# Performance work log

Measured on AMD Instinct MI355X. Metric: run time of the kernel, lower is better.

The kernel has to match this reference:

```python
import jax, jax.numpy as jnp
import numpy as np

B, L, P, K, D, H = 8192, 224, 6, 5, 128, 4
S = K * K                 # 25 spatial positions in the patch
CENTER = S // 2           # central target pixel index
SCALE_RANGE = 0.2
BN_EPS = 1e-5


def _uniform(k, shape, fan_in):
    s = 1.0 / np.sqrt(fan_in)
    return jax.random.uniform(k, shape, jnp.float32, -s, s)


def setup_inputs() -> dict:
    key = jax.random.key(0)
    ks = jax.random.split(key, 32)
    inp = {}
    inp["x"] = jax.random.normal(ks[0], (B, L, K, K), jnp.float32)
    # attention projections (stored as (in, out), applied as x @ W + b)
    inp["wk_w"] = _uniform(ks[1], (L, D), L); inp["wk_b"] = _uniform(ks[2], (D,), L)
    inp["wv_w"] = _uniform(ks[3], (L, D), L); inp["wv_b"] = _uniform(ks[4], (D,), L)
    inp["wq_w"] = _uniform(ks[5], (L, D), L); inp["wq_b"] = _uniform(ks[6], (D,), L)
    inp["ng_w"] = _uniform(ks[7], (D, 1), D); inp["ng_b"] = _uniform(ks[8], (1,), D)
    # ffn branch: GLU(128->64) -> BN -> GLU(64->P)
    inp["f1_fw"] = _uniform(ks[9], (D, 64), D);  inp["f1_fb"] = _uniform(ks[10], (64,), D)
    inp["f1_gw"] = _uniform(ks[11], (D, 64), D); inp["f1_gb"] = _uniform(ks[12], (64,), D)
    inp["f_bn_g"] = jnp.ones((64,), jnp.float32); inp["f_bn_b"] = jnp.zeros((64,), jnp.float32)
    inp["f2_fw"] = _uniform(ks[13], (64, P), 64); inp["f2_fb"] = _uniform(ks[14], (P,), 64)
    inp["f2_gw"] = _uniform(ks[15], (64, P), 64); inp["f2_gb"] = _uniform(ks[16], (P,), 64)
    # scalar branch: same shapes
    inp["s1_fw"] = _uniform(ks[17], (D, 64), D);  inp["s1_fb"] = _uniform(ks[18], (64,), D)
    inp["s1_gw"] = _uniform(ks[19], (D, 64), D);  inp["s1_gb"] = _uniform(ks[20], (64,), D)
    inp["s_bn_g"] = jnp.ones((64,), jnp.float32); inp["s_bn_b"] = jnp.zeros((64,), jnp.float32)
    inp["s2_fw"] = _uniform(ks[21], (64, P), 64); inp["s2_fb"] = _uniform(ks[22], (P,), 64)
    inp["s2_gw"] = _uniform(ks[23], (64, P), 64); inp["s2_gb"] = _uniform(ks[24], (P,), 64)
    # endmember spectra (P, L), nonnegative as typical for HSI
    inp["endmember"] = jax.random.uniform(ks[25], (P, L), jnp.float32)
    return inp


def _swish(x):
    return x * jax.nn.sigmoid(x)


def _glu(x, fw, fb, gw, gb):
    return (x @ fw + fb) * jax.nn.sigmoid(x @ gw + gb)


def _bn_train(x, g, b):
    # BatchNorm1d training-mode forward: biased batch stats over batch dim
    m = jnp.mean(x, axis=0)
    v = jnp.var(x, axis=0)
    return (x - m) * jax.lax.rsqrt(v + BN_EPS) * g + b


def _forward(x, wk_w, wk_b, wv_w, wv_b, wq_w, wq_b, ng_w, ng_b,
             f1_fw, f1_fb, f1_gw, f1_gb, f_bn_g, f_bn_b, f2_fw, f2_fb, f2_gw, f2_gb,
             s1_fw, s1_fb, s1_gw, s1_gb, s_bn_g, s_bn_b, s2_fw, s2_fb, s2_gw, s2_gb,
             endmember):
    b = x.shape[0]
    xt = x.reshape(b, L, S).transpose(0, 2, 1)        # (B, S, L)
    keys = xt @ wk_w + wk_b                            # (B, S, D)
    vals = xt @ wv_w + wv_b                            # (B, S, D)
    q = xt[:, CENTER] @ wq_w + wq_b                    # (B, D)
    dk, dv = D // H, D // H
    kh = keys.reshape(b, S, H, dk)
    qh = q.reshape(b, H, dk)
    # note: scaling uses full key_dim (np.sqrt(self.key_dim)), not per-head dim
    scores = jnp.einsum('bhd,bshd->bhs', qh, kh) / np.sqrt(D).astype(np.float32)
    mask = jnp.zeros((S,), jnp.float32).at[CENTER].set(-1e6)
    att = jax.nn.softmax(scores + mask, axis=-1)       # (B, H, S)
    vh = vals.reshape(b, S, H, dv)
    surround = jnp.einsum('bhs,bshd->bhd', att, vh).reshape(b, D)
    central = vals[:, CENTER]                          # (B, D)
    nearby = jax.nn.sigmoid((central - surround) @ ng_w + ng_b)  # (B, 1)
    ss = central + nearby * surround                   # (B, D) spatial-spectral feature

    h = _glu(_swish(ss), f1_fw, f1_fb, f1_gw, f1_gb)
    h = _swish(_bn_train(h, f_bn_g, f_bn_b))
    abd = jax.nn.softmax(_glu(h, f2_fw, f2_fb, f2_gw, f2_gb), axis=1)  # (B, P)

    g = _glu(_swish(ss), s1_fw, s1_fb, s1_gw, s1_gb)
    g = _swish(_bn_train(g, s_bn_g, s_bn_b))
    edm_scale = jnp.tanh(_glu(g, s2_fw, s2_fb, s2_gw, s2_gb))          # (B, P)

    scale = 1.0 + SCALE_RANGE * edm_scale[:, :, None]  # (B, P, 1)
    edm = scale * endmember[None]                      # (B, P, L)
    recon = jnp.einsum('bp,bpl->bl', abd, edm)         # (B, L)
    return recon, abd, edm_scale


def reference(x, wk_w, wk_b, wv_w, wv_b, wq_w, wq_b, ng_w, ng_b,
              f1_fw, f1_fb, f1_gw, f1_gb, f_bn_g, f_bn_b, f2_fw, f2_fb, f2_gw, f2_gb,
              s1_fw, s1_fb, s1_gw, s1_gb, s_bn_g, s_bn_b, s2_fw, s2_fb, s2_gw, s2_gb,
              endmember):
    return _forward(x, wk_w, wk_b, wv_w, wv_b, wq_w, wq_b, ng_w, ng_b,
                    f1_fw, f1_fb, f1_gw, f1_gb, f_bn_g, f_bn_b, f2_fw, f2_fb, f2_gw, f2_gb,
                    s1_fw, s1_fb, s1_gw, s1_gb, s_bn_g, s_bn_b, s2_fw, s2_fb, s2_gw, s2_gb,
                    endmember)
```

## Files before the change

kernel.cpp:

```cpp
#include <hip/hip_runtime.h>
#include <hip/hip_bf16.h>

typedef unsigned short ushort;
typedef unsigned int   uint;
typedef __bf16 bfrag_t __attribute__((ext_vector_type(8)));
typedef float  ffrag_t __attribute__((ext_vector_type(4)));

#define NB   8192
#define LL   224
#define SS   25
#define CTR  12
#define DD   128
#define PP   6
#define HID  64
#define GPB  2
#define NKC  7
#define NMT  4
#define NNT  24
#define VST  132
#define WPK_ELEMS (NKC * NNT * 64 * 8)
#define FC1_ELEMS (4 * 16 * 64 * 8)

__device__ __forceinline__ float f_sigmoid(float x) { return 1.0f / (1.0f + __expf(-x)); }
__device__ __forceinline__ ushort f2bf(float f) {
    __hip_bfloat16 h = __float2bfloat16(f);
    ushort u; __builtin_memcpy(&u, &h, 2); return u;
}
__device__ __forceinline__ float bfu2f(ushort u) {
    uint v = ((uint)u) << 16; float f; __builtin_memcpy(&f, &v, 4); return f;
}

__global__ __launch_bounds__(256) void k0_pack(
    const float* __restrict__ wk_w, const float* __restrict__ wv_w,
    const float* __restrict__ wq_w,
    const float* __restrict__ f1_fw, const float* __restrict__ f1_gw,
    const float* __restrict__ s1_fw, const float* __restrict__ s1_gw,
    ushort* __restrict__ wpack, ushort* __restrict__ fc1pack,
    float* __restrict__ stats)
{
    const int blk = blockIdx.x;
    if (blk == 0) stats[threadIdx.x] = 0.f;
    if (blk < NNT) {
        const int nt  = blk;
        const int mat = nt >> 3;
        const float* w = mat == 0 ? wk_w : (mat == 1 ? wv_w : wq_w);
        const int cb = (nt & 7) * 16;
        for (int e = threadIdx.x; e < NKC * 64 * 8; e += 256) {
            int j    = e & 7;
            int lane = (e >> 3) & 63;
            int kc   = e >> 9;
            int k = kc * 32 + ((lane >> 4) << 3) + j;
            int c = cb + (lane & 15);
            wpack[((kc * NNT + nt) * 64 + lane) * 8 + j] = f2bf(w[k * DD + c]);
        }
    } else {
        const int nt = blk - NNT;
        const int m2 = nt >> 2;
        const float* w = m2 == 0 ? f1_fw : (m2 == 1 ? f1_gw : (m2 == 2 ? s1_fw : s1_gw));
        const int cb = (nt & 3) * 16;
        for (int e = threadIdx.x; e < 4 * 64 * 8; e += 256) {
            int j    = e & 7;
            int lane = (e >> 3) & 63;
            int kc   = e >> 9;
            int k = kc * 32 + ((lane >> 4) << 3) + j;
            int c = cb + (lane & 15);
            fc1pack[((kc * 16 + nt) * 64 + lane) * 8 + j] = f2bf(w[k * HID + c]);
        }
    }
}

__global__ __launch_bounds__(512, 4) void kA_front(
    const float* __restrict__ x,
    const ushort* __restrict__ wpack,
    const float* __restrict__ wk_b, const float* __restrict__ wv_b,
    const float* __restrict__ wq_b,
    const float* __restrict__ ng_w, const float* __restrict__ ng_b,
    ushort* __restrict__ swv_ws)
{
    __shared__ ushort alds[NMT * NKC * 64 * 8];
    __shared__ float  qv[GPB * DD];
    __shared__ float  att[8 * 26];
    __shared__ float  red[4];

    const int t    = threadIdx.x;
    const int b0   = blockIdx.x * GPB;
    const int wave = t >> 6;
    const int lane = t & 63;

    const int cC = wave * 16 + (lane & 15);
    const float biask = wk_b[cC];
    const float biasv = wv_b[cC];
    const float biasq = wq_b[cC];
    const float ngw   = ng_w[t & 127];

    const float4* xb4 = (const float4*)(x + (size_t)b0 * (LL * SS));
    float4 xf[6];
#pragma unroll
    for (int k = 0; k < 6; ++k) {
        int q = t + k * 512;
        if (q < 2800) xf[k] = xb4[q];
    }
#pragma unroll
    for (int k = 0; k < 6; ++k) {
        int q = t + k * 512;
        if (q < 2800) {
            int e0 = q * 4;
            int g  = e0 >= 5600;
            int eb0 = e0 - g * 5600;
#pragma unroll
            for (int c = 0; c < 4; ++c) {
                int eb = eb0 + c;
                int l = eb / 25;
                int s = eb - l * 25;
                int r = g * 32 + s;
                int idx = (((r >> 4) * NKC + (l >> 5)) * 64 +
                           ((r & 15) | (((l >> 3) & 3) << 4))) * 8 + (l & 7);
                float fv = c == 0 ? xf[k].x : c == 1 ? xf[k].y : c == 2 ? xf[k].z : xf[k].w;
                alds[idx] = f2bf(fv);
            }
        }
    }
    __syncthreads();

    ffrag_t acck[NMT], accv[NMT], accq[2];
#pragma unroll
    for (int mt = 0; mt < NMT; ++mt) {
        acck[mt] = ffrag_t{0.f, 0.f, 0.f, 0.f};
        accv[mt] = ffrag_t{0.f, 0.f, 0.f, 0.f};
    }
    accq[0] = ffrag_t{0.f, 0.f, 0.f, 0.f};
    accq[1] = ffrag_t{0.f, 0.f, 0.f, 0.f};

    bfrag_t bk = *(const bfrag_t*)(wpack + ((0 * NNT + wave) * 64 + lane) * 8);
    bfrag_t bv = *(const bfrag_t*)(wpack + ((0 * NNT + wave + 8) * 64 + lane) * 8);
    bfrag_t bq = *(const bfrag_t*)(wpack + ((0 * NNT + wave + 16) * 64 + lane) * 8);
#pragma unroll
    for (int kc = 0; kc < NKC; ++kc) {
        bfrag_t nbk, nbv, nbq;
        if (kc + 1 < NKC) {
            nbk = *(const bfrag_t*)(wpack + (((kc + 1) * NNT + wave) * 64 + lane) * 8);
            nbv = *(const bfrag_t*)(wpack + (((kc + 1) * NNT + wave + 8) * 64 + lane) * 8);
            nbq = *(const bfrag_t*)(wpack + (((kc + 1) * NNT + wave + 16) * 64 + lane) * 8);
        }
#pragma unroll
        for (int mt = 0; mt < NMT; ++mt) {
            bfrag_t af = *(const bfrag_t*)(alds + ((mt * NKC + kc) * 64 + lane) * 8);
            acck[mt] = __builtin_amdgcn_mfma_f32_16x16x32_bf16(af, bk, acck[mt], 0, 0, 0);
            accv[mt] = __builtin_amdgcn_mfma_f32_16x16x32_bf16(af, bv, accv[mt], 0, 0, 0);
            if ((mt & 1) == 0)
                accq[mt >> 1] = __builtin_amdgcn_mfma_f32_16x16x32_bf16(af, bq, accq[mt >> 1], 0, 0, 0);
        }
        if (kc + 1 < NKC) { bk = nbk; bv = nbv; bq = nbq; }
    }
    __syncthreads();

    {
#pragma unroll
        for (int mt = 0; mt < NMT; ++mt) {
#pragma unroll
            for (int reg = 0; reg < 4; ++reg) {
                int r = mt * 16 + ((lane >> 4) << 2) + reg;
                int g = r >> 5;
                int s = r & 31;
                if (s < SS) {
                    alds[(g * SS + s) * VST + cC]        = f2bf(acck[mt][reg] + biask);
                    alds[6600 + (g * SS + s) * VST + cC] = f2bf(accv[mt][reg] + biasv);
                }
            }
        }
        if ((lane >> 4) == 3) {
            qv[cC]      = accq[0][0] + biasq;
            qv[DD + cC] = accq[1][0] + biasq;
        }
    }
    __syncthreads();

    if (t < 256) {
        const int r   = t >> 5;
        const int g   = r >> 2;
        const int h   = r & 3;
        const int l32 = t & 31;
        float sc = -1e30f;
        if (l32 < SS) {
            const ushort* kr = alds + (g * SS + l32) * VST + h * 32;
            const float*  qr = qv + g * DD + h * 32;
            float a0 = 0.f, a1 = 0.f, a2 = 0.f, a3 = 0.f;
#pragma unroll
            for (int i = 0; i < 32; i += 4) {
                a0 = fmaf(qr[i + 0], bfu2f(kr[i + 0]), a0);
                a1 = fmaf(qr[i + 1], bfu2f(kr[i + 1]), a1);
                a2 = fmaf(qr[i + 2], bfu2f(kr[i + 2]), a2);
                a3 = fmaf(qr[i + 3], bfu2f(kr[i + 3]), a3);
            }
            sc = ((a0 + a1) + (a2 + a3)) * 0.088388347648318447f;
            if (l32 == CTR) sc -= 1e6f;
        }
        float mx = sc;
#pragma unroll
        for (int m = 16; m > 0; m >>= 1) mx = fmaxf(mx, __shfl_xor(mx, m, 32));
        float e = __expf(sc - mx);
        float sum = e;
#pragma unroll
        for (int m = 16; m > 0; m >>= 1) sum += __shfl_xor(sum, m, 32);
        if (l32 < SS) att[r * 26 + l32] = e / sum;
    }
    __syncthreads();

    if (t < 256) {
        const int g = t >> 7;
        const int d = t & 127;
        const int h = d >> 5;
        const ushort* vrow = alds + 6600 + g * SS * VST + d;
        const float* arow = att + (g * 4 + h) * 26;
        float s0 = 0.f, s1 = 0.f;
#pragma unroll
        for (int s = 0; s < 24; s += 2) {
            s0 = fmaf(arow[s],     bfu2f(vrow[s * VST]),       s0);
            s1 = fmaf(arow[s + 1], bfu2f(vrow[(s + 1) * VST]), s1);
        }
        float sur = fmaf(arow[24], bfu2f(vrow[24 * VST]), s0 + s1);
        float cen = bfu2f(vrow[CTR * VST]);
        float term = (cen - sur) * ngw;
#pragma unroll
        for (int off = 32; off > 0; off >>= 1) term += __shfl_down(term, off);
        if (lane == 0) red[wave] = term;
        __syncthreads();
        float tot = red[g * 2] + red[g * 2 + 1] + ng_b[0];
        float nearby = f_sigmoid(tot);
        float ssv = cen + nearby * sur;
        float sw  = ssv * f_sigmoid(ssv);
        swv_ws[(size_t)(b0 + g) * DD + d] = f2bf(sw);
    } else {
        __syncthreads();
    }
}

__global__ __launch_bounds__(256) void kC_fc1(
    const ushort* __restrict__ swv_ws,
    const ushort* __restrict__ fc1pack,
    const float* __restrict__ f1_fb, const float* __restrict__ f1_gb,
    const float* __restrict__ s1_fb, const float* __restrict__ s1_gb,
    float* __restrict__ h1_ws, float* __restrict__ g1_ws,
    float* __restrict__ stats)
{
    const int t    = threadIdx.x;
    const int wave = t >> 6;
    const int lane = t & 63;
    const int m0   = blockIdx.x * 32;
    const int c16  = wave * 16 + (lane & 15);

    const float fb1 = f1_fb[c16], gb1 = f1_gb[c16];
    const float fb2 = s1_fb[c16], gb2 = s1_gb[c16];

    ffrag_t acc[4][2];
#pragma unroll
    for (int ni = 0; ni < 4; ++ni)
#pragma unroll
        for (int mt = 0; mt < 2; ++mt) acc[ni][mt] = ffrag_t{0.f, 0.f, 0.f, 0.f};

#pragma unroll
    for (int kc = 0; kc < 4; ++kc) {
        bfrag_t bf[4];
#pragma unroll
        for (int ni = 0; ni < 4; ++ni) {
            int nt = wave + 4 * ni;
            bf[ni] = *(const bfrag_t*)(fc1pack + ((kc * 16 + nt) * 64 + lane) * 8);
        }
#pragma unroll
        for (int mt = 0; mt < 2; ++mt) {
            bfrag_t af = *(const bfrag_t*)(swv_ws +
                (size_t)(m0 + mt * 16 + (lane & 15)) * DD + kc * 32 + ((lane >> 4) << 3));
#pragma unroll
            for (int ni = 0; ni < 4; ++ni)
                acc[ni][mt] = __builtin_amdgcn_mfma_f32_16x16x32_bf16(af, bf[ni], acc[ni][mt], 0, 0, 0);
        }
    }

    float hs = 0.f, hq = 0.f, gs = 0.f, gq = 0.f;
#pragma unroll
    for (int mt = 0; mt < 2; ++mt) {
#pragma unroll
        for (int reg = 0; reg < 4; ++reg) {
            int m = m0 + mt * 16 + ((lane >> 4) << 2) + reg;
            float hv = (acc[0][mt][reg] + fb1) * f_sigmoid(acc[1][mt][reg] + gb1);
            float gv = (acc[2][mt][reg] + fb2) * f_sigmoid(acc[3][mt][reg] + gb2);
            h1_ws[(size_t)m * HID + c16] = hv;
            g1_ws[(size_t)m * HID + c16] = gv;
            hs += hv; hq = fmaf(hv, hv, hq);
            gs += gv; gq = fmaf(gv, gv, gq);
        }
    }
    hs += __shfl_xor(hs, 16); hs += __shfl_xor(hs, 32);
    hq += __shfl_xor(hq, 16); hq += __shfl_xor(hq, 32);
    gs += __shfl_xor(gs, 16); gs += __shfl_xor(gs, 32);
    gq += __shfl_xor(gq, 16); gq += __shfl_xor(gq, 32);
    const int cg = lane >> 4;
    float val = cg == 0 ? hs : cg == 1 ? hq : cg == 2 ? gs : gq;
    atomicAdd(&stats[cg * 64 + c16], val);
}

#define K3G 32
__global__ __launch_bounds__(256) void k3_back(
    const float* __restrict__ h1, const float* __restrict__ g1,
    const float* __restrict__ stats,
    const float* __restrict__ f_bng, const float* __restrict__ f_bnb,
    const float* __restrict__ s_bng, const float* __restrict__ s_bnb,
    const float* __restrict__ f2_fw, const float* __restrict__ f2_fb,
    const float* __restrict__ f2_gw, const float* __restrict__ f2_gb,
    const float* __restrict__ s2_fw, const float* __restrict__ s2_fb,
    const float* __restrict__ s2_gw, const float* __restrict__ s2_gb,
    const float* __restrict__ endm,
    float* __restrict__ out_recon, float* __restrict__ out_abd,
    float* __restrict__ out_es)
{
    const int B0 = blockIdx.x * K3G;
    const int t = threadIdx.x;
    __shared__ float bnl[256];
    __shared__ float w2[4][HID * PP];
    __shared__ float b2[4][8];
    __shared__ float endl[PP * LL];
    __shared__ float hh[K3G * 65], gg[K3G * 65];
    __shared__ float logit[K3G * 8], esv[K3G * 8], coef[K3G * 8];

    if (t < 128) {
        int br = t >> 6, j = t & 63;
        float S1 = stats[br * 128 + j];
        float S2 = stats[br * 128 + 64 + j];
        float m   = S1 * (1.0f / NB);
        float var = S2 * (1.0f / NB) - m * m;
        float gam = br ? s_bng[j] : f_bng[j];
        float be  = br ? s_bnb[j] : f_bnb[j];
        float a   = gam * rsqrtf(var + 1e-5f);
        bnl[br * 128 + j]      = a;
        bnl[br * 128 + 64 + j] = be - m * a;
    }
    for (int i = t; i < HID * PP; i += 256) {
        w2[0][i] = f2_fw[i];
        w2[1][i] = f2_gw[i];
        w2[2][i] = s2_fw[i];
        w2[3][i] = s2_gw[i];
    }
    if (t < PP) {
        b2[0][t] = f2_fb[t];
        b2[1][t] = f2_gb[t];
        b2[2][t] = s2_fb[t];
        b2[3][t] = s2_gb[t];
    }
    for (int i = t; i < PP * LL; i += 256) endl[i] = endm[i];
    __syncthreads();

    for (int i = t; i < K3G * HID; i += 256) {
        int ba = i >> 6, j = i & 63;
        float v1 = h1[(size_t)(B0 + ba) * HID + j] * bnl[j] + bnl[64 + j];
        hh[ba * 65 + j] = v1 * f_sigmoid(v1);
        float v2 = g1[(size_t)(B0 + ba) * HID + j] * bnl[128 + j] + bnl[192 + j];
        gg[ba * 65 + j] = v2 * f_sigmoid(v2);
    }
    __syncthreads();

    for (int i = t; i < K3G * 2 * PP; i += 256) {
        int ba = i / (2 * PP);
        int rr = i - ba * (2 * PP);
        int br = rr / PP;
        int p  = rr - br * PP;
        const float* src = (br ? gg : hh) + ba * 65;
        const float* fw  = w2[br * 2];
        const float* gw  = w2[br * 2 + 1];
        float df = b2[br * 2][p], dg = b2[br * 2 + 1][p];
#pragma unroll 8
        for (int j = 0; j < HID; ++j) {
            float v = src[j];
            df = fmaf(v, fw[j * PP + p], df);
            dg = fmaf(v, gw[j * PP + p], dg);
        }
        float glu = df * f_sigmoid(dg);
        if (br == 0) {
            logit[ba * 8 + p] = glu;
        } else {
            float e = tanhf(glu);
            esv[ba * 8 + p] = e;
            out_es[(size_t)(B0 + ba) * PP + p] = e;
        }
    }
    __syncthreads();

    if (t < K3G) {
        float mx = -1e30f;
#pragma unroll
        for (int p = 0; p < PP; ++p) mx = fmaxf(mx, logit[t * 8 + p]);
        float e[PP]; float sum = 0.f;
#pragma unroll
        for (int p = 0; p < PP; ++p) { e[p] = __expf(logit[t * 8 + p] - mx); sum += e[p]; }
        float inv = 1.0f / sum;
#pragma unroll
        for (int p = 0; p < PP; ++p) {
            float a = e[p] * inv;
            out_abd[(size_t)(B0 + t) * PP + p] = a;
            coef[t * 8 + p] = a * (1.0f + 0.2f * esv[t * 8 + p]);
        }
    }
    __syncthreads();

    for (int i = t; i < K3G * LL; i += 256) {
        int ba = i / LL;
        int l  = i - ba * LL;
        float r = 0.f;
#pragma unroll
        for (int p = 0; p < PP; ++p)
            r = fmaf(coef[ba * 8 + p], endl[p * LL + l], r);
        out_recon[(size_t)(B0 + ba) * LL + l] = r;
    }
}

extern "C" void kernel_launch(void* const* d_in, const int* in_sizes, int n_in,
                              void* d_out, int out_size, void* d_ws, size_t ws_size,
                              hipStream_t stream)
{
    const float* x     = (const float*)d_in[0];
    const float* wk_w  = (const float*)d_in[1];
    const float* wk_b  = (const float*)d_in[2];
    const float* wv_w  = (const float*)d_in[3];
    const float* wv_b  = (const float*)d_in[4];
    const float* wq_w  = (const float*)d_in[5];
    const float* wq_b  = (const float*)d_in[6];
    const float* ng_w  = (const float*)d_in[7];
    const float* ng_b  = (const float*)d_in[8];
    const float* f1_fw = (const float*)d_in[9];
    const float* f1_fb = (const float*)d_in[10];
    const float* f1_gw = (const float*)d_in[11];
    const float* f1_gb = (const float*)d_in[12];
    const float* f_bng = (const float*)d_in[13];
    const float* f_bnb = (const float*)d_in[14];
    const float* f2_fw = (const float*)d_in[15];
    const float* f2_fb = (const float*)d_in[16];
    const float* f2_gw = (const float*)d_in[17];
    const float* f2_gb = (const float*)d_in[18];
    const float* s1_fw = (const float*)d_in[19];
    const float* s1_fb = (const float*)d_in[20];
    const float* s1_gw = (const float*)d_in[21];
    const float* s1_gb = (const float*)d_in[22];
    const float* s_bng = (const float*)d_in[23];
    const float* s_bnb = (const float*)d_in[24];
    const float* s2_fw = (const float*)d_in[25];
    const float* s2_fb = (const float*)d_in[26];
    const float* s2_gw = (const float*)d_in[27];
    const float* s2_gb = (const float*)d_in[28];
    const float* endm  = (const float*)d_in[29];

    float* ws = (float*)d_ws;
    float*  h1_ws   = ws;
    float*  g1_ws   = ws + (size_t)NB * HID;
    float*  stats   = ws + 1048576;
    ushort* wpack   = (ushort*)(ws + 1048832);
    ushort* fc1pack = (ushort*)(ws + 1048832 + WPK_ELEMS / 2);
    ushort* swv_ws  = (ushort*)(ws + 1048832 + (WPK_ELEMS + FC1_ELEMS) / 2);

    float* out       = (float*)d_out;
    float* out_recon = out;
    float* out_abd   = out + (size_t)NB * LL;
    float* out_es    = out + (size_t)NB * (LL + PP);

    k0_pack<<<NNT + 16, 256, 0, stream>>>(wk_w, wv_w, wq_w, f1_fw, f1_gw,
                                          s1_fw, s1_gw, wpack, fc1pack, stats);
    kA_front<<<NB / GPB, 512, 0, stream>>>(x, wpack, wk_b, wv_b, wq_b,
                                           ng_w, ng_b, swv_ws);
    kC_fc1<<<NB / 32, 256, 0, stream>>>(swv_ws, fc1pack, f1_fb, f1_gb,
                                        s1_fb, s1_gb, h1_ws, g1_ws, stats);
    k3_back<<<NB / K3G, 256, 0, stream>>>(h1_ws, g1_ws, stats,
                                          f_bng, f_bnb, s_bng, s_bnb,
                                          f2_fw, f2_fb, f2_gw, f2_gb,
                                          s2_fw, s2_fb, s2_gw, s2_gb,
                                          endm, out_recon, out_abd, out_es);
}
```

Baseline: 370.2 us.

## Fuse FC1 GLU into front kernel and process four pixels per block

Moves the first GLU layer (128->64 for both branches) into the attention front kernel, so the swished features stay in shared memory instead of going through a global bf16 workspace and a separate kC_fc1 launch. The front kernel now handles four pixels per block, which doubles the M tiles for the QKV MFMAs and lets all 512 threads do attention work. The fused FC1 uses MFMA tiles with only 4 valid rows out of 16, and each block issues its own batch-statistics atomics. k3_back's group size is also halved, and the larger register and LDS footprint could reduce occupancy.

```diff
diff --git a/kernel.cpp b/kernel.cpp
--- a/kernel.cpp
+++ b/kernel.cpp
@@ -13,11 +13,12 @@
 #define DD   128
 #define PP   6
 #define HID  64
-#define GPB  2
+#define GPB  4
 #define NKC  7
-#define NMT  4
+#define NMT  8
 #define NNT  24
 #define VST  132
+#define VBASE (GPB * SS * VST)
 #define WPK_ELEMS (NKC * NNT * 64 * 8)
 #define FC1_ELEMS (4 * 16 * 64 * 8)
 
@@ -72,15 +73,20 @@
 __global__ __launch_bounds__(512, 4) void kA_front(
     const float* __restrict__ x,
     const ushort* __restrict__ wpack,
+    const ushort* __restrict__ fc1pack,
     const float* __restrict__ wk_b, const float* __restrict__ wv_b,
     const float* __restrict__ wq_b,
     const float* __restrict__ ng_w, const float* __restrict__ ng_b,
-    ushort* __restrict__ swv_ws)
+    const float* __restrict__ f1_fb, const float* __restrict__ f1_gb,
+    const float* __restrict__ s1_fb, const float* __restrict__ s1_gb,
+    float* __restrict__ h1_ws, float* __restrict__ g1_ws,
+    float* __restrict__ stats)
 {
     __shared__ ushort alds[NMT * NKC * 64 * 8];
     __shared__ float  qv[GPB * DD];
-    __shared__ float  att[8 * 26];
-    __shared__ float  red[4];
+    __shared__ float  att[16 * 26];
+    __shared__ float  red[8];
+    __shared__ ushort swl[GPB * DD];
 
     const int t    = threadIdx.x;
     const int b0   = blockIdx.x * GPB;
@@ -94,18 +100,18 @@
     const float ngw   = ng_w[t & 127];
 
     const float4* xb4 = (const float4*)(x + (size_t)b0 * (LL * SS));
-    float4 xf[6];
-#pragma unroll
-    for (int k = 0; k < 6; ++k) {
+    float4 xf[11];
+#pragma unroll
+    for (int k = 0; k < 11; ++k) {
         int q = t + k * 512;
-        if (q < 2800) xf[k] = xb4[q];
-    }
-#pragma unroll
-    for (int k = 0; k < 6; ++k) {
+        if (q < 5600) xf[k] = xb4[q];
+    }
+#pragma unroll
+    for (int k = 0; k < 11; ++k) {
         int q = t + k * 512;
-        if (q < 2800) {
-            int e0 = q * 4;
-            int g  = e0 >= 5600;
+        if (q < 5600) {
+            int g   = q / 1400;
+            int e0  = q * 4;
             int eb0 = e0 - g * 5600;
 #pragma unroll
             for (int c = 0; c < 4; ++c) {
@@ -122,14 +128,14 @@
     }
     __syncthreads();
 
-    ffrag_t acck[NMT], accv[NMT], accq[2];
+    ffrag_t acck[NMT], accv[NMT], accq[4];
 #pragma unroll
     for (int mt = 0; mt < NMT; ++mt) {
         acck[mt] = ffrag_t{0.f, 0.f, 0.f, 0.f};
         accv[mt] = ffrag_t{0.f, 0.f, 0.f, 0.f};
     }
-    accq[0] = ffrag_t{0.f, 0.f, 0.f, 0.f};
-    accq[1] = ffrag_t{0.f, 0.f, 0.f, 0.f};
+#pragma unroll
+    for (int i = 0; i < 4; ++i) accq[i] = ffrag_t{0.f, 0.f, 0.f, 0.f};
 
     bfrag_t bk = *(const bfrag_t*)(wpack + ((0 * NNT + wave) * 64 + lane) * 8);
     bfrag_t bv = *(const bfrag_t*)(wpack + ((0 * NNT + wave + 8) * 64 + lane) * 8);
@@ -163,19 +169,21 @@
                 int g = r >> 5;
                 int s = r & 31;
                 if (s < SS) {
-                    alds[(g * SS + s) * VST + cC]        = f2bf(acck[mt][reg] + biask);
-                    alds[6600 + (g * SS + s) * VST + cC] = f2bf(accv[mt][reg] + biasv);
+                    alds[(g * SS + s) * VST + cC]         = f2bf(acck[mt][reg] + biask);
+                    alds[VBASE + (g * SS + s) * VST + cC] = f2bf(accv[mt][reg] + biasv);
                 }
             }
         }
         if ((lane >> 4) == 3) {
-            qv[cC]      = accq[0][0] + biasq;
-            qv[DD + cC] = accq[1][0] + biasq;
-        }
-    }
-    __syncthreads();
-
-    if (t < 256) {
+            qv[cC]           = accq[0][0] + biasq;
+            qv[DD + cC]      = accq[1][0] + biasq;
+            qv[2 * DD + cC]  = accq[2][0] + biasq;
+            qv[3 * DD + cC]  = accq[3][0] + biasq;
+        }
+    }
+    __syncthreads();
+
+    {
         const int r   = t >> 5;
         const int g   = r >> 2;
         const int h   = r & 3;
@@ -206,11 +214,11 @@
     }
     __syncthreads();
 
-    if (t < 256) {
+    {
         const int g = t >> 7;
         const int d = t & 127;
         const int h = d >> 5;
-        const ushort* vrow = alds + 6600 + g * SS * VST + d;
+        const ushort* vrow = alds + VBASE + g * SS * VST + d;
         const float* arow = att + (g * 4 + h) * 26;
         float s0 = 0.f, s1 = 0.f;
 #pragma unroll
@@ -229,77 +237,44 @@
         float nearby = f_sigmoid(tot);
         float ssv = cen + nearby * sur;
         float sw  = ssv * f_sigmoid(ssv);
-        swv_ws[(size_t)(b0 + g) * DD + d] = f2bf(sw);
-    } else {
-        __syncthreads();
-    }
-}
-
-__global__ __launch_bounds__(256) void kC_fc1(
-    const ushort* __restrict__ swv_ws,
-    const ushort* __restrict__ fc1pack,
-    const float* __restrict__ f1_fb, const float* __restrict__ f1_gb,
-    const float* __restrict__ s1_fb, const float* __restrict__ s1_gb,
-    float* __restrict__ h1_ws, float* __restrict__ g1_ws,
-    float* __restrict__ stats)
-{
-    const int t    = threadIdx.x;
-    const int wave = t >> 6;
-    const int lane = t & 63;
-    const int m0   = blockIdx.x * 32;
-    const int c16  = wave * 16 + (lane & 15);
-
-    const float fb1 = f1_fb[c16], gb1 = f1_gb[c16];
-    const float fb2 = s1_fb[c16], gb2 = s1_gb[c16];
-
-    ffrag_t acc[4][2];
-#pragma unroll
-    for (int ni = 0; ni < 4; ++ni)
-#pragma unroll
-        for (int mt = 0; mt < 2; ++mt) acc[ni][mt] = ffrag_t{0.f, 0.f, 0.f, 0.f};
-
-#pragma unroll
-    for (int kc = 0; kc < 4; ++kc) {
-        bfrag_t bf[4];
-#pragma unroll
-        for (int ni = 0; ni < 4; ++ni) {
-            int nt = wave + 4 * ni;
-            bf[ni] = *(const bfrag_t*)(fc1pack + ((kc * 16 + nt) * 64 + lane) * 8);
-        }
-#pragma unroll
-        for (int mt = 0; mt < 2; ++mt) {
-            bfrag_t af = *(const bfrag_t*)(swv_ws +
-                (size_t)(m0 + mt * 16 + (lane & 15)) * DD + kc * 32 + ((lane >> 4) << 3));
-#pragma unroll
-            for (int ni = 0; ni < 4; ++ni)
-                acc[ni][mt] = __builtin_amdgcn_mfma_f32_16x16x32_bf16(af, bf[ni], acc[ni][mt], 0, 0, 0);
-        }
-    }
-
-    float hs = 0.f, hq = 0.f, gs = 0.f, gq = 0.f;
-#pragma unroll
-    for (int mt = 0; mt < 2; ++mt) {
-#pragma unroll
-        for (int reg = 0; reg < 4; ++reg) {
-            int m = m0 + mt * 16 + ((lane >> 4) << 2) + reg;
-            float hv = (acc[0][mt][reg] + fb1) * f_sigmoid(acc[1][mt][reg] + gb1);
-            float gv = (acc[2][mt][reg] + fb2) * f_sigmoid(acc[3][mt][reg] + gb2);
-            h1_ws[(size_t)m * HID + c16] = hv;
-            g1_ws[(size_t)m * HID + c16] = gv;
-            hs += hv; hq = fmaf(hv, hv, hq);
-            gs += gv; gq = fmaf(gv, gv, gq);
-        }
-    }
-    hs += __shfl_xor(hs, 16); hs += __shfl_xor(hs, 32);
-    hq += __shfl_xor(hq, 16); hq += __shfl_xor(hq, 32);
-    gs += __shfl_xor(gs, 16); gs += __shfl_xor(gs, 32);
-    gq += __shfl_xor(gq, 16); gq += __shfl_xor(gq, 32);
-    const int cg = lane >> 4;
-    float val = cg == 0 ? hs : cg == 1 ? hq : cg == 2 ? gs : gq;
-    atomicAdd(&stats[cg * 64 + c16], val);
-}
-
-#define K3G 32
+        swl[g * DD + d] = f2bf(sw);
+    }
+    __syncthreads();
+
+    {
+        const int path = wave >> 2;
+        const int cg   = wave & 3;
+        const int ntf  = path * 8 + cg;
+        const int ntg  = ntf + 4;
+        ffrag_t accf = ffrag_t{0.f, 0.f, 0.f, 0.f};
+        ffrag_t accg = ffrag_t{0.f, 0.f, 0.f, 0.f};
+#pragma unroll
+        for (int kc = 0; kc < 4; ++kc) {
+            bfrag_t av = *(const bfrag_t*)(swl + (lane & 3) * DD + kc * 32 + ((lane >> 4) << 3));
+            bfrag_t bf = *(const bfrag_t*)(fc1pack + ((kc * 16 + ntf) * 64 + lane) * 8);
+            bfrag_t bg = *(const bfrag_t*)(fc1pack + ((kc * 16 + ntg) * 64 + lane) * 8);
+            accf = __builtin_amdgcn_mfma_f32_16x16x32_bf16(av, bf, accf, 0, 0, 0);
+            accg = __builtin_amdgcn_mfma_f32_16x16x32_bf16(av, bg, accg, 0, 0, 0);
+        }
+        if ((lane >> 4) == 0) {
+            const int c = cg * 16 + (lane & 15);
+            const float fb = path ? s1_fb[c] : f1_fb[c];
+            const float gb = path ? s1_gb[c] : f1_gb[c];
+            float* dst = path ? g1_ws : h1_ws;
+            float sum = 0.f, sq = 0.f;
+#pragma unroll
+            for (int reg = 0; reg < 4; ++reg) {
+                float v = (accf[reg] + fb) * f_sigmoid(accg[reg] + gb);
+                dst[(size_t)(b0 + reg) * HID + c] = v;
+                sum += v; sq = fmaf(v, v, sq);
+            }
+            atomicAdd(&stats[path * 128 + c], sum);
+            atomicAdd(&stats[path * 128 + 64 + c], sq);
+        }
+    }
+}
+
+#define K3G 16
 __global__ __launch_bounds__(256) void k3_back(
     const float* __restrict__ h1, const float* __restrict__ g1,
     const float* __restrict__ stats,
@@ -453,7 +428,6 @@
     float*  stats   = ws + 1048576;
     ushort* wpack   = (ushort*)(ws + 1048832);
     ushort* fc1pack = (ushort*)(ws + 1048832 + WPK_ELEMS / 2);
-    ushort* swv_ws  = (ushort*)(ws + 1048832 + (WPK_ELEMS + FC1_ELEMS) / 2);
 
     float* out       = (float*)d_out;
     float* out_recon = out;
@@ -462,10 +436,10 @@
 
     k0_pack<<<NNT + 16, 256, 0, stream>>>(wk_w, wv_w, wq_w, f1_fw, f1_gw,
                                           s1_fw, s1_gw, wpack, fc1pack, stats);
-    kA_front<<<NB / GPB, 512, 0, stream>>>(x, wpack, wk_b, wv_b, wq_b,
-                                           ng_w, ng_b, swv_ws);
-    kC_fc1<<<NB / 32, 256, 0, stream>>>(swv_ws, fc1pack, f1_fb, f1_gb,
-                                        s1_fb, s1_gb, h1_ws, g1_ws, stats);
+    kA_front<<<NB / GPB, 512, 0, stream>>>(x, wpack, fc1pack,
+                                           wk_b, wv_b, wq_b, ng_w, ng_b,
+                                           f1_fb, f1_gb, s1_fb, s1_gb,
+                                           h1_ws, g1_ws, stats);
     k3_back<<<NB / K3G, 256, 0, stream>>>(h1_ws, g1_ws, stats,
                                           f_bng, f_bnb, s_bng, s_bnb,
                                           f2_fw, f2_fb, f2_gw, f2_gb,
```

New measurement: 374.6 us. Within noise of the previous version (+1.2%).
